# Optimization experiments

Measured on AMD Instinct MI355X. Metric: run time of the kernel, lower is better.

## Reference

```python
import jax, jax.numpy as jnp
import numpy as np

V, D, H, L, T_CTX = 50257, 768, 12, 12, 1024
HD = D // H
GELU_C = float(np.sqrt(2.0 / np.pi))


def new_gelu(x):
    return 0.5 * x * (1.0 + jnp.tanh(GELU_C * (x + 0.044715 * x ** 3)))


def layernorm(x, w, b, eps=1e-5):
    mu = jnp.mean(x, axis=-1, keepdims=True)
    var = jnp.var(x, axis=-1, keepdims=True)
    return (x - mu) * jax.lax.rsqrt(var + eps) * w + b


def setup_inputs() -> dict:
    key = jax.random.key(0)
    ks = jax.random.split(key, 20)
    B, T = 2, 1024
    s = 0.02
    inp = {
        "idx": jax.random.randint(ks[0], (B, T), 0, V),
        "targets": jax.random.randint(ks[1], (B, T), 0, V),
        "wte": jax.random.normal(ks[2], (V, D), jnp.float32) * s,
        "wpe": jax.random.normal(ks[3], (T_CTX, D), jnp.float32) * s,
        "ln1_w": jnp.ones((L, D)), "ln1_b": jnp.zeros((L, D)),
        "qkv_w": jax.random.normal(ks[4], (L, D, 3 * D), jnp.float32) * s,
        "qkv_b": jnp.zeros((L, 3 * D)),
        "proj_w": jax.random.normal(ks[5], (L, D, D), jnp.float32) * s,
        "proj_b": jnp.zeros((L, D)),
        "ln2_w": jnp.ones((L, D)), "ln2_b": jnp.zeros((L, D)),
        "fc_w": jax.random.normal(ks[6], (L, D, 4 * D), jnp.float32) * s,
        "fc_b": jnp.zeros((L, 4 * D)),
        "fc2_w": jax.random.normal(ks[7], (L, 4 * D, D), jnp.float32) * s,
        "fc2_b": jnp.zeros((L, D)),
        "lnf_w": jnp.ones((D,)), "lnf_b": jnp.zeros((D,)),
    }
    return inp


def _gpt_forward(idx, targets, wte, wpe, ln1_w, ln1_b, qkv_w, qkv_b, proj_w,
                 proj_b, ln2_w, ln2_b, fc_w, fc_b, fc2_w, fc2_b, lnf_w, lnf_b):
    B, T = idx.shape
    x = wte[idx] + wpe[:T]  # [B,T,D]
    scale = 1.0 / np.sqrt(HD)
    causal = jnp.tril(jnp.ones((T, T), dtype=bool))

    def block(x, p):
        l1w, l1b, qw, qb, pw, pb, l2w, l2b, fw, fb, f2w, f2b = p
        h = layernorm(x, l1w, l1b)
        qkv = h @ qw + qb  # [B,T,3D]
        q, k, v = jnp.split(qkv, 3, axis=-1)
        q = q.reshape(B, T, H, HD).transpose(0, 2, 1, 3)
        k = k.reshape(B, T, H, HD).transpose(0, 2, 1, 3)
        v = v.reshape(B, T, H, HD).transpose(0, 2, 1, 3)
        attn = jnp.einsum('bhqd,bhkd->bhqk', q, k) * scale
        attn = jnp.where(causal, attn, -jnp.inf)
        attn = jax.nn.softmax(attn, axis=-1)
        o = jnp.einsum('bhqk,bhkd->bhqd', attn, v)
        o = o.transpose(0, 2, 1, 3).reshape(B, T, D)
        x = x + (o @ pw + pb)
        h = layernorm(x, l2w, l2b)
        h = new_gelu(h @ fw + fb) @ f2w + f2b
        return x + h, None

    params = (ln1_w, ln1_b, qkv_w, qkv_b, proj_w, proj_b,
              ln2_w, ln2_b, fc_w, fc_b, fc2_w, fc2_b)
    x, _ = jax.lax.scan(block, x, params)
    x = layernorm(x, lnf_w, lnf_b)
    logits = x @ wte.T  # tied lm_head, [B,T,V]

    logp = jax.nn.log_softmax(logits, axis=-1)
    tflat = targets.reshape(-1)
    valid = tflat != -1
    tsafe = jnp.where(valid, tflat, 0)
    nll = -jnp.take_along_axis(logp.reshape(-1, V), tsafe[:, None], axis=-1)[:, 0]
    loss = jnp.sum(jnp.where(valid, nll, 0.0)) / jnp.maximum(jnp.sum(valid), 1)
    return logits, loss


def reference(idx, targets, wte, wpe, ln1_w, ln1_b, qkv_w, qkv_b, proj_w,
              proj_b, ln2_w, ln2_b, fc_w, fc_b, fc2_w, fc2_b, lnf_w, lnf_b):
    return _gpt_forward(idx, targets, wte, wpe, ln1_w, ln1_b, qkv_w, qkv_b,
                        proj_w, proj_b, ln2_w, ln2_b, fc_w, fc_b, fc2_w, fc2_b,
                        lnf_w, lnf_b)
```

## Files before the change

### kernel.cpp

```cpp
#include <hip/hip_runtime.h>
#include <hip/hip_bf16.h>
#include <math.h>

#define TT 1024
#define BB 2
#define DD 768
#define HH 12
#define NHD 64
#define LL 12
#define VV 50257
#define MROWS (BB*TT)
#define VPAD 50304

typedef __attribute__((ext_vector_type(4))) float f32x4;
typedef __attribute__((ext_vector_type(8))) __bf16 bf16x8;
typedef __attribute__((ext_vector_type(8))) unsigned short u16x8;
typedef __hip_bfloat16 bf16;

__device__ __forceinline__ void gload_lds16(const bf16* g, bf16* l) {
    __builtin_amdgcn_global_load_lds((const __attribute__((address_space(1))) void*)g,
                                     (__attribute__((address_space(3))) void*)l, 16, 0, 0);
}

__global__ void embed_kernel(const int* __restrict__ idx, const float* __restrict__ wte,
                             const float* __restrict__ wpe, float* __restrict__ x) {
    int m = blockIdx.x;
    int t = m % TT;
    int tok = idx[m];
    const float* wrow = wte + (size_t)tok * DD;
    const float* prow = wpe + (size_t)t * DD;
    float* xrow = x + (size_t)m * DD;
    for (int c = threadIdx.x; c < DD; c += blockDim.x)
        xrow[c] = wrow[c] + prow[c];
}

__global__ void ln_kernel(const float* __restrict__ x, const float* __restrict__ w,
                          const float* __restrict__ b, bf16* __restrict__ out) {
    __shared__ float red[256];
    int m = blockIdx.x;
    int tid = threadIdx.x;
    const float* xr = x + (size_t)m * DD;
    float v0 = xr[tid], v1 = xr[tid + 256], v2 = xr[tid + 512];
    red[tid] = v0 + v1 + v2;
    __syncthreads();
    for (int s = 128; s > 0; s >>= 1) { if (tid < s) red[tid] += red[tid + s]; __syncthreads(); }
    float mu = red[0] * (1.0f / DD);
    __syncthreads();
    float d0 = v0 - mu, d1 = v1 - mu, d2 = v2 - mu;
    red[tid] = d0 * d0 + d1 * d1 + d2 * d2;
    __syncthreads();
    for (int s = 128; s > 0; s >>= 1) { if (tid < s) red[tid] += red[tid + s]; __syncthreads(); }
    float rstd = rsqrtf(red[0] * (1.0f / DD) + 1e-5f);
    bf16* orow = out + (size_t)m * DD;
    orow[tid]       = __float2bfloat16(d0 * rstd * w[tid]       + b[tid]);
    orow[tid + 256] = __float2bfloat16(d1 * rstd * w[tid + 256] + b[tid + 256]);
    orow[tid + 512] = __float2bfloat16(d2 * rstd * w[tid + 512] + b[tid + 512]);
}

__global__ void cast_kernel(const float* __restrict__ src, bf16* __restrict__ dst, int n4) {
    int stride = gridDim.x * blockDim.x;
    for (int i = blockIdx.x * blockDim.x + threadIdx.x; i < n4; i += stride) {
        float4 v = *(const float4*)(src + (size_t)i * 4);
        bf16* d = dst + (size_t)i * 4;
        d[0] = __float2bfloat16(v.x); d[1] = __float2bfloat16(v.y);
        d[2] = __float2bfloat16(v.z); d[3] = __float2bfloat16(v.w);
    }
}

__global__ void tcast_kernel(const float* __restrict__ W, bf16* __restrict__ Wt,
                             int K, int N, size_t wstride, size_t tstride) {
    W  += (size_t)blockIdx.z * wstride;
    Wt += (size_t)blockIdx.z * tstride;
    __shared__ float t[32][33];
    int n0 = blockIdx.x * 32, k0 = blockIdx.y * 32;
    int c = threadIdx.x & 31, g = threadIdx.x >> 5;
    #pragma unroll
    for (int i = 0; i < 4; ++i) {
        int k = g * 4 + i;
        t[k][c] = W[(size_t)(k0 + k) * N + n0 + c];
    }
    __syncthreads();
    #pragma unroll
    for (int i = 0; i < 4; ++i) {
        int n = g * 4 + i;
        Wt[(size_t)(n0 + n) * K + k0 + c] = __float2bfloat16(t[c][n]);
    }
}

template<int BM, int BN, bool BIAS, bool GELU_, bool RES, bool OUTBF16, bool NCHECK, bool SPLITK>
__global__ __launch_bounds__(256, 3) void mgemm(
        const bf16* __restrict__ A, const bf16* __restrict__ Bm,
        const float* __restrict__ bias, const float* __restrict__ res,
        float* __restrict__ Cf, bf16* __restrict__ Cb, int M, int N, int K) {
    constexpr int WM = BM / 32, WN = BN / 32;
    constexpr int RA = BM / 64, RB = BN / 64;
    constexpr int NL = RA + RB;
    __shared__ __align__(16) bf16 As[2][BM * 32];
    __shared__ __align__(16) bf16 Bs[2][BN * 32];
    const int tid = threadIdx.x, lane = tid & 63, wid = tid >> 6;
    const int nbx = gridDim.x;
    const int nwg = nbx * gridDim.y;
    const int bidl = blockIdx.x + nbx * blockIdx.y;
    const int cpx = nwg >> 3;
    const int sw = (bidl & 7) * cpx + (bidl >> 3);
    const int m0 = (sw % nbx) * BM, n0 = (sw / nbx) * BN;
    const int wr = (wid >> 1) * (BM / 2), wc = (wid & 1) * (BN / 2);
    const int fr = lane & 15, fq = lane >> 4;

    const int Keff  = SPLITK ? (K >> 1) : K;
    const int kbase = SPLITK ? blockIdx.z * Keff : 0;
    if (SPLITK) Cf += (size_t)blockIdx.z * M * N;

    const int ksrc = ((lane & 3) ^ ((lane >> 3) & 3)) * 8;
    const bf16* gA = A  + (size_t)(m0 + wid * 16 + (lane >> 2)) * K + kbase + ksrc;
    const bf16* gB = Bm + (size_t)(n0 + wid * 16 + (lane >> 2)) * K + kbase + ksrc;
    bf16* lA = &As[0][0] + wid * 512 + lane * 8;
    bf16* lB = &Bs[0][0] + wid * 512 + lane * 8;
    const int kph = (fq ^ ((fr >> 1) & 3)) * 8;

    f32x4 acc[WM][WN] = {};
    const int nt = Keff / 32;

    #pragma unroll
    for (int i = 0; i < RA; ++i) gload_lds16(gA + (size_t)(i * 64) * K, lA + i * 2048);
    #pragma unroll
    for (int i = 0; i < RB; ++i) gload_lds16(gB + (size_t)(i * 64) * K, lB + i * 2048);

    for (int t = 0; t < nt; ++t) {
        const int cur = t & 1;
        if (t + 1 < nt) {
            const bf16* pA = gA + (t + 1) * 32;
            const bf16* pB = gB + (t + 1) * 32;
            bf16* dA = lA + (cur ^ 1) * (BM * 32);
            bf16* dB = lB + (cur ^ 1) * (BN * 32);
            #pragma unroll
            for (int i = 0; i < RA; ++i) gload_lds16(pA + (size_t)(i * 64) * K, dA + i * 2048);
            #pragma unroll
            for (int i = 0; i < RB; ++i) gload_lds16(pB + (size_t)(i * 64) * K, dB + i * 2048);
            asm volatile("s_waitcnt vmcnt(%0)" :: "i"(NL) : "memory");
        } else {
            asm volatile("s_waitcnt vmcnt(0)" ::: "memory");
        }
        __builtin_amdgcn_s_barrier();
        __builtin_amdgcn_sched_barrier(0);
        const bf16* abase = &As[cur][0];
        const bf16* bbase = &Bs[cur][0];
        bf16x8 af[WM], bq[WN];
        #pragma unroll
        for (int m = 0; m < WM; ++m)
            af[m] = *(const bf16x8*)(abase + (wr + m * 16 + fr) * 32 + kph);
        #pragma unroll
        for (int n = 0; n < WN; ++n)
            bq[n] = *(const bf16x8*)(bbase + (wc + n * 16 + fr) * 32 + kph);
        #pragma unroll
        for (int m = 0; m < WM; ++m)
            #pragma unroll
            for (int n = 0; n < WN; ++n)
                acc[m][n] = __builtin_amdgcn_mfma_f32_16x16x32_bf16(af[m], bq[n], acc[m][n], 0, 0, 0);
        __builtin_amdgcn_sched_barrier(0);
        __builtin_amdgcn_s_barrier();
    }

    #pragma unroll
    for (int m = 0; m < WM; ++m) {
        const int row = m0 + wr + m * 16 + fq * 4;
        #pragma unroll
        for (int n = 0; n < WN; ++n) {
            const int col = n0 + wc + n * 16 + fr;
            if (NCHECK && col >= N) continue;
            float bv = BIAS ? bias[col] : 0.f;
            #pragma unroll
            for (int r = 0; r < 4; ++r) {
                float v = acc[m][n][r] + bv;
                if (GELU_) {
                    float u = v;
                    v = 0.5f * u * (1.0f + tanhf(0.7978845608028654f * (u + 0.044715f * u * u * u)));
                }
                if (RES) v += res[(size_t)(row + r) * N + col];
                if (OUTBF16) Cb[(size_t)(row + r) * N + col] = __float2bfloat16(v);
                else         Cf[(size_t)(row + r) * N + col] = v;
            }
        }
    }
}

__global__ void red_kernel(const float* __restrict__ part, const float* __restrict__ bias,
                           float* __restrict__ x) {
    const size_t MN = (size_t)MROWS * DD;
    size_t i = ((size_t)blockIdx.x * blockDim.x + threadIdx.x) * 4;
    float4 p0 = *(const float4*)(part + i);
    float4 p1 = *(const float4*)(part + MN + i);
    float4 xv = *(const float4*)(x + i);
    float4 bv = *(const float4*)(bias + (int)(i % DD));
    xv.x += p0.x + p1.x + bv.x;
    xv.y += p0.y + p1.y + bv.y;
    xv.z += p0.z + p1.z + bv.z;
    xv.w += p0.w + p1.w + bv.w;
    *(float4*)(x + i) = xv;
}

__global__ __launch_bounds__(256) void attn3_kernel(const bf16* __restrict__ qkv,
                                                    bf16* __restrict__ out) {
    __shared__ bf16 Vt[64 * 64];
    __shared__ bf16 Ps[4][16 * 64];
    const int bid = blockIdx.x;
    const int q0 = (15 - (bid & 15)) * 64;
    const int h  = (bid / (TT / 64)) % HH;
    const int b  = bid / ((TT / 64) * HH);
    const int tid = threadIdx.x, lane = tid & 63, wid = tid >> 6;
    const int fr = lane & 15, fq = lane >> 4;
    const size_t rs = 3 * DD;

    bf16x8 qf[2];
    {
        const bf16* qb = qkv + (size_t)(b * TT + q0 + wid * 16 + fr) * rs + h * NHD;
        qf[0] = *(const bf16x8*)(qb + fq * 8);
        qf[1] = *(const bf16x8*)(qb + 32 + fq * 8);
    }
    float mrun[4] = {-1e30f, -1e30f, -1e30f, -1e30f};
    float lrun[4] = {0.f, 0.f, 0.f, 0.f};
    f32x4 o[4] = {};
    const int vrow = (tid & 31) * 2, kq = tid >> 5;
    const int ntile = q0 / 64 + 1;

    for (int jt = 0; jt < ntile; ++jt) {
        __syncthreads();
        {
            const u16x8* vb = (const u16x8*)(qkv + (size_t)(b * TT + jt * 64 + vrow) * rs + 2 * DD + h * NHD + kq * 8);
            u16x8 v0 = vb[0];
            u16x8 v1 = *(const u16x8*)((const bf16*)vb + rs);
            #pragma unroll
            for (int j = 0; j < 8; ++j) {
                int d = kq * 8 + j;
                int e = (d * 64 + vrow) ^ ((d & 7) << 3);
                *(unsigned int*)&Vt[e] = (unsigned int)v0[j] | ((unsigned int)v1[j] << 16);
            }
        }
        f32x4 s[4] = {};
        const bf16* kb = qkv + (size_t)(b * TT + jt * 64 + fr) * rs + DD + h * NHD;
        __builtin_amdgcn_s_setprio(1);
        #pragma unroll
        for (int n = 0; n < 4; ++n) {
            bf16x8 k0 = *(const bf16x8*)(kb + (size_t)(n * 16) * rs + fq * 8);
            bf16x8 k1 = *(const bf16x8*)(kb + (size_t)(n * 16) * rs + 32 + fq * 8);
            s[n] = __builtin_amdgcn_mfma_f32_16x16x32_bf16(qf[0], k0, s[n], 0, 0, 0);
            s[n] = __builtin_amdgcn_mfma_f32_16x16x32_bf16(qf[1], k1, s[n], 0, 0, 0);
        }
        __builtin_amdgcn_s_setprio(0);
        float mt[4] = {-1e30f, -1e30f, -1e30f, -1e30f};
        #pragma unroll
        for (int n = 0; n < 4; ++n) {
            int colg = jt * 64 + n * 16 + fr;
            #pragma unroll
            for (int r = 0; r < 4; ++r) {
                int rowg = q0 + wid * 16 + fq * 4 + r;
                float v = s[n][r] * 0.125f;
                if (colg > rowg) v = -1e30f;
                s[n][r] = v;
                mt[r] = fmaxf(mt[r], v);
            }
        }
        #pragma unroll
        for (int msk = 1; msk <= 8; msk <<= 1)
            #pragma unroll
            for (int r = 0; r < 4; ++r) mt[r] = fmaxf(mt[r], __shfl_xor(mt[r], msk));
        float sc[4], pt[4] = {0.f, 0.f, 0.f, 0.f};
        #pragma unroll
        for (int r = 0; r < 4; ++r) {
            float mn = fmaxf(mrun[r], mt[r]);
            sc[r] = __expf(mrun[r] - mn);
            mrun[r] = mn;
        }
        #pragma unroll
        for (int n = 0; n < 4; ++n)
            #pragma unroll
            for (int r = 0; r < 4; ++r) {
                float p = __expf(s[n][r] - mrun[r]);
                s[n][r] = p;
                pt[r] += p;
            }
        #pragma unroll
        for (int msk = 1; msk <= 8; msk <<= 1)
            #pragma unroll
            for (int r = 0; r < 4; ++r) pt[r] += __shfl_xor(pt[r], msk);
        #pragma unroll
        for (int r = 0; r < 4; ++r) lrun[r] = lrun[r] * sc[r] + pt[r];
        #pragma unroll
        for (int n2 = 0; n2 < 4; ++n2)
            #pragma unroll
            for (int r = 0; r < 4; ++r) o[n2][r] *= sc[r];
        #pragma unroll
        for (int n = 0; n < 4; ++n)
            #pragma unroll
            for (int r = 0; r < 4; ++r) {
                int row = fq * 4 + r;
                int e = (row * 64 + n * 16 + fr) ^ ((row & 7) << 3);
                Ps[wid][e] = __float2bfloat16(s[n][r]);
            }
        __syncthreads();
        __builtin_amdgcn_s_setprio(1);
        #pragma unroll
        for (int ks = 0; ks < 2; ++ks) {
            int pe = (fr * 64 + ks * 32 + fq * 8) ^ ((fr & 7) << 3);
            bf16x8 pa = *(const bf16x8*)&Ps[wid][pe];
            #pragma unroll
            for (int n2 = 0; n2 < 4; ++n2) {
                int d = n2 * 16 + fr;
                int ve = (d * 64 + ks * 32 + fq * 8) ^ ((d & 7) << 3);
                bf16x8 vv = *(const bf16x8*)&Vt[ve];
                o[n2] = __builtin_amdgcn_mfma_f32_16x16x32_bf16(pa, vv, o[n2], 0, 0, 0);
            }
        }
        __builtin_amdgcn_s_setprio(0);
    }
    #pragma unroll
    for (int r = 0; r < 4; ++r) {
        float inv = 1.f / lrun[r];
        bf16* op = out + (size_t)(b * TT + q0 + wid * 16 + fq * 4 + r) * DD + h * NHD;
        #pragma unroll
        for (int n2 = 0; n2 < 4; ++n2)
            op[n2 * 16 + fr] = __float2bfloat16(o[n2][r] * inv);
    }
}

__global__ void zero_kernel(float* p) { if (threadIdx.x == 0) p[0] = 0.f; }

__device__ __forceinline__ void ol_push(float v, float& mx, float& sm) {
    if (v > mx) { sm *= __expf(mx - v); mx = v; }
    sm += __expf(v - mx);
}

__global__ void loss_kernel(const float* __restrict__ logits, const int* __restrict__ targets,
                            float* __restrict__ acc) {
    __shared__ float rm[256], rs[256];
    int m = blockIdx.x;
    int tid = threadIdx.x;
    const float* lr = logits + (size_t)m * VV;
    const int lead = (4 - (m & 3)) & 3;
    const int nv = (VV - lead) >> 2;
    float mx = -1e30f, sm = 0.f;
    if (tid < lead) ol_push(lr[tid], mx, sm);
    const float4* lr4 = (const float4*)(lr + lead);
    for (int i = tid; i < nv; i += 256) {
        float4 v = lr4[i];
        ol_push(v.x, mx, sm); ol_push(v.y, mx, sm);
        ol_push(v.z, mx, sm); ol_push(v.w, mx, sm);
    }
    for (int i = lead + 4 * nv + tid; i < VV; i += 256) ol_push(lr[i], mx, sm);
    rm[tid] = mx; rs[tid] = sm;
    __syncthreads();
    for (int s = 128; s > 0; s >>= 1) {
        if (tid < s) {
            float m2 = rm[tid + s], s2 = rs[tid + s];
            float nm = fmaxf(rm[tid], m2);
            rs[tid] = rs[tid] * __expf(rm[tid] - nm) + s2 * __expf(m2 - nm);
            rm[tid] = nm;
        }
        __syncthreads();
    }
    if (tid == 0) {
        float lse = logf(rs[0]) + rm[0];
        atomicAdd(acc, lse - lr[targets[m]]);
    }
}

__global__ void loss_final(const float* __restrict__ acc, float* __restrict__ out) {
    if (threadIdx.x == 0) out[0] = acc[0] * (1.0f / (float)MROWS);
}

extern "C" void kernel_launch(void* const* d_in, const int* in_sizes, int n_in,
                              void* d_out, int out_size, void* d_ws, size_t ws_size,
                              hipStream_t stream) {
    const int*   idx     = (const int*)d_in[0];
    const int*   targets = (const int*)d_in[1];
    const float* wte     = (const float*)d_in[2];
    const float* wpe     = (const float*)d_in[3];
    const float* ln1_w   = (const float*)d_in[4];
    const float* ln1_b   = (const float*)d_in[5];
    const float* qkv_w   = (const float*)d_in[6];
    const float* qkv_b   = (const float*)d_in[7];
    const float* proj_w  = (const float*)d_in[8];
    const float* proj_b  = (const float*)d_in[9];
    const float* ln2_w   = (const float*)d_in[10];
    const float* ln2_b   = (const float*)d_in[11];
    const float* fc_w    = (const float*)d_in[12];
    const float* fc_b    = (const float*)d_in[13];
    const float* fc2_w   = (const float*)d_in[14];
    const float* fc2_b   = (const float*)d_in[15];
    const float* lnf_w   = (const float*)d_in[16];
    const float* lnf_b   = (const float*)d_in[17];

    float* logits = (float*)d_out;
    float* loss_out = logits + (size_t)MROWS * VV;

    const size_t LQ = (size_t)3 * DD * DD, LP = (size_t)DD * DD;
    const size_t LF = (size_t)4 * DD * DD, LF2 = (size_t)4 * DD * DD;
    const size_t LSTRIDE = LQ + LP + LF + LF2;

    float* x    = (float*)d_ws;
    float* lacc = x + (size_t)MROWS * DD;
    float* part = lacc + 16;
    bf16* qkvbuf = (bf16*)(part + (size_t)2 * MROWS * DD);
    bf16* hb   = qkvbuf + (size_t)MROWS * 3 * DD;
    bf16* ab   = hb + (size_t)MROWS * DD;
    bf16* gb   = ab + (size_t)MROWS * DD;
    bf16* wteb = gb + (size_t)MROWS * 4 * DD;
    bf16* wbase = wteb + (size_t)VPAD * DD;

    const size_t fixed_bytes = (size_t)((char*)wbase - (char*)d_ws);
    const bool hoist = ws_size >= fixed_bytes + sizeof(bf16) * LSTRIDE * LL;

    dim3 blk(256);
    cast_kernel<<<2048, blk, 0, stream>>>(wte, wteb, VV * DD / 4);
    embed_kernel<<<MROWS, blk, 0, stream>>>(idx, wte, wpe, x);

    if (hoist) {
        tcast_kernel<<<dim3(3 * DD / 32, DD / 32, LL), blk, 0, stream>>>(
            qkv_w, wbase, DD, 3 * DD, LQ, LSTRIDE);
        tcast_kernel<<<dim3(DD / 32, DD / 32, LL), blk, 0, stream>>>(
            proj_w, wbase + LQ, DD, DD, LP, LSTRIDE);
        tcast_kernel<<<dim3(4 * DD / 32, DD / 32, LL), blk, 0, stream>>>(
            fc_w, wbase + LQ + LP, DD, 4 * DD, LF, LSTRIDE);
        tcast_kernel<<<dim3(DD / 32, 4 * DD / 32, LL), blk, 0, stream>>>(
            fc2_w, wbase + LQ + LP + LF, 4 * DD, DD, LF2, LSTRIDE);
    }

    const int nred = (MROWS * DD) / (4 * 256);

    for (int l = 0; l < LL; ++l) {
        bf16* wl = hoist ? wbase + (size_t)l * LSTRIDE : wbase;
        bf16* wQT = wl, *wPT = wl + LQ, *wFT = wl + LQ + LP, *wF2T = wl + LQ + LP + LF;
        if (!hoist) {
            tcast_kernel<<<dim3(3 * DD / 32, DD / 32, 1), blk, 0, stream>>>(qkv_w + (size_t)l * LQ, wQT, DD, 3 * DD, 0, 0);
            tcast_kernel<<<dim3(DD / 32, DD / 32, 1), blk, 0, stream>>>(proj_w + (size_t)l * LP, wPT, DD, DD, 0, 0);
            tcast_kernel<<<dim3(4 * DD / 32, DD / 32, 1), blk, 0, stream>>>(fc_w + (size_t)l * LF, wFT, DD, 4 * DD, 0, 0);
            tcast_kernel<<<dim3(DD / 32, 4 * DD / 32, 1), blk, 0, stream>>>(fc2_w + (size_t)l * LF2, wF2T, 4 * DD, DD, 0, 0);
        }

        ln_kernel<<<MROWS, blk, 0, stream>>>(x, ln1_w + (size_t)l * DD, ln1_b + (size_t)l * DD, hb);

        mgemm<128, 128, true, false, false, true, false, false><<<dim3(MROWS / 128, 3 * DD / 128), blk, 0, stream>>>(
            hb, wQT, qkv_b + (size_t)l * 3 * DD, nullptr, nullptr, qkvbuf, MROWS, 3 * DD, DD);

        attn3_kernel<<<BB * HH * (TT / 64), blk, 0, stream>>>(qkvbuf, ab);

        mgemm<64, 64, false, false, false, false, false, true><<<dim3(MROWS / 64, DD / 64, 2), blk, 0, stream>>>(
            ab, wPT, nullptr, nullptr, part, nullptr, MROWS, DD, DD);
        red_kernel<<<nred, blk, 0, stream>>>(part, proj_b + (size_t)l * DD, x);

        ln_kernel<<<MROWS, blk, 0, stream>>>(x, ln2_w + (size_t)l * DD, ln2_b + (size_t)l * DD, hb);

        mgemm<128, 128, true, true, false, true, false, false><<<dim3(MROWS / 128, 4 * DD / 128), blk, 0, stream>>>(
            hb, wFT, fc_b + (size_t)l * 4 * DD, nullptr, nullptr, gb, MROWS, 4 * DD, DD);

        mgemm<64, 64, false, false, false, false, false, true><<<dim3(MROWS / 64, DD / 64, 2), blk, 0, stream>>>(
            gb, wF2T, nullptr, nullptr, part, nullptr, MROWS, DD, 4 * DD);
        red_kernel<<<nred, blk, 0, stream>>>(part, fc2_b + (size_t)l * DD, x);
    }

    ln_kernel<<<MROWS, blk, 0, stream>>>(x, lnf_w, lnf_b, hb);

    mgemm<128, 128, false, false, false, false, true, false><<<dim3(MROWS / 128, VPAD / 128), blk, 0, stream>>>(
        hb, wteb, nullptr, nullptr, logits, nullptr, MROWS, VV, DD);

    zero_kernel<<<1, 64, 0, stream>>>(lacc);
    loss_kernel<<<MROWS, blk, 0, stream>>>(logits, targets, lacc);
    loss_final<<<1, 64, 0, stream>>>(lacc, loss_out);
}
```

Before: 2.567 ms.

## Use 256x256-tile double-buffered MFMA GEMM with XCD swizzle for lm_head

Replaces the 128x128 generic GEMM for the tied lm_head projection with a dedicated 512-thread, 256x256-tile kernel. It uses swizzled LDS layout, direct global-to-LDS loads interleaved between MFMA groups, setprio, and a block-index remap that groups workgroups by XCD. The vocab padding grows to a multiple of 256, and the pad rows are zeroed by a new kernel. The aim is higher arithmetic intensity and better MFMA utilisation on the largest GEMM, at the cost of heavier LDS use (128KB per block) and more complex manual waitcnt scheduling.

```diff
diff --git a/kernel.cpp b/kernel.cpp
--- a/kernel.cpp
+++ b/kernel.cpp
@@ -10,7 +10,7 @@
 #define LL 12
 #define VV 50257
 #define MROWS (BB*TT)
-#define VPAD 50304
+#define NPAD 50432
 
 typedef __attribute__((ext_vector_type(4))) float f32x4;
 typedef __attribute__((ext_vector_type(8))) __bf16 bf16x8;
@@ -67,6 +67,11 @@
     }
 }
 
+__global__ void padzero_kernel(bf16* __restrict__ p, int n) {
+    int i = blockIdx.x * 256 + threadIdx.x;
+    if (i < n) p[i] = __float2bfloat16(0.f);
+}
+
 __global__ void tcast_kernel(const float* __restrict__ W, bf16* __restrict__ Wt,
                              int K, int N, size_t wstride, size_t tstride) {
     W  += (size_t)blockIdx.z * wstride;
@@ -179,6 +184,94 @@
                 if (RES) v += res[(size_t)(row + r) * N + col];
                 if (OUTBF16) Cb[(size_t)(row + r) * N + col] = __float2bfloat16(v);
                 else         Cf[(size_t)(row + r) * N + col] = v;
+            }
+        }
+    }
+}
+
+template<int K>
+__global__ __launch_bounds__(512, 2) void mgemm256(
+        const bf16* __restrict__ A, const bf16* __restrict__ Bm,
+        float* __restrict__ Cf, int N) {
+    __shared__ __align__(16) bf16 As[2][256 * 64];
+    __shared__ __align__(16) bf16 Bs[2][256 * 64];
+    const int tid = threadIdx.x, lane = tid & 63, wid = tid >> 6;
+    const int wm = wid >> 2, wn = wid & 3;
+    const int fr = lane & 15, fq = lane >> 4;
+    const int nbx = gridDim.x;
+    const int nwg = nbx * gridDim.y;
+    const int bidl = blockIdx.x + nbx * blockIdx.y;
+    const int cpx = nwg >> 3;
+    const int sw = (bidl & 7) * cpx + (bidl >> 3);
+    const int m0 = (sw % nbx) * 256, n0 = (sw / nbx) * 256;
+
+    const int srow = tid >> 3;
+    const int ksw  = ((tid & 7) ^ (srow & 7)) * 8;
+    const int nt = K / 64;
+    const int swl = fr & 7;
+
+    f32x4 acc[8][4] = {};
+
+#define STA(T, U) gload_lds16(A  + (size_t)(m0 + (U)*64 + srow) * K + (T)*64 + ksw, \
+                              &As[(T) & 1][0] + (U)*4096 + tid*8)
+#define STB(T, U) gload_lds16(Bm + (size_t)(n0 + (U)*64 + srow) * K + (T)*64 + ksw, \
+                              &Bs[(T) & 1][0] + (U)*4096 + tid*8)
+#define LDA(DST, M_, KS) DST = *(const bf16x8*)(ab + (wm*128 + (M_)*16 + fr)*64 + ((((KS)*4+fq) ^ swl)*8))
+#define LDB(DST, N_, KS) DST = *(const bf16x8*)(bb + (wn*64  + (N_)*16 + fr)*64 + ((((KS)*4+fq) ^ swl)*8))
+#define MFMA16(Q) { bf16x8 a0, a1, a2, a3;                                         \
+        LDA(a0, 2*(Q),   0); LDA(a1, 2*(Q),   1);                                  \
+        LDA(a2, 2*(Q)+1, 0); LDA(a3, 2*(Q)+1, 1);                                  \
+        __builtin_amdgcn_s_setprio(1);                                             \
+        _Pragma("unroll")                                                          \
+        for (int n = 0; n < 4; ++n) {                                              \
+            acc[2*(Q)][n]   = __builtin_amdgcn_mfma_f32_16x16x32_bf16(a0, bq[n][0], acc[2*(Q)][n], 0, 0, 0);   \
+            acc[2*(Q)][n]   = __builtin_amdgcn_mfma_f32_16x16x32_bf16(a1, bq[n][1], acc[2*(Q)][n], 0, 0, 0);   \
+            acc[2*(Q)+1][n] = __builtin_amdgcn_mfma_f32_16x16x32_bf16(a2, bq[n][0], acc[2*(Q)+1][n], 0, 0, 0); \
+            acc[2*(Q)+1][n] = __builtin_amdgcn_mfma_f32_16x16x32_bf16(a3, bq[n][1], acc[2*(Q)+1][n], 0, 0, 0); \
+        }                                                                          \
+        __builtin_amdgcn_s_setprio(0); }
+
+    STA(0,0); STA(0,1); STA(0,2); STA(0,3); STB(0,0); STB(0,1); STB(0,2); STB(0,3);
+    STA(1,0); STA(1,1); STA(1,2); STA(1,3); STB(1,0); STB(1,1); STB(1,2); STB(1,3);
+
+    #pragma unroll 1
+    for (int t = 0; t < nt; ++t) {
+        const bf16* ab = &As[t & 1][0];
+        const bf16* bb = &Bs[t & 1][0];
+        if (t + 1 < nt) asm volatile("s_waitcnt vmcnt(6)" ::: "memory");
+        else            asm volatile("s_waitcnt vmcnt(0)" ::: "memory");
+        __builtin_amdgcn_s_barrier();
+        if (t >= 1 && t + 1 < nt) { STA(t+1, 1); STA(t+1, 3); }
+        bf16x8 bq[4][2];
+        #pragma unroll
+        for (int n = 0; n < 4; ++n) { LDB(bq[n][0], n, 0); LDB(bq[n][1], n, 1); }
+        MFMA16(0)
+        __builtin_amdgcn_s_barrier();
+        if (t + 2 < nt) { STB(t+2, 0); STB(t+2, 1); }
+        MFMA16(1)
+        __builtin_amdgcn_s_barrier();
+        if (t + 2 < nt) { STB(t+2, 2); STB(t+2, 3); STA(t+2, 0); STA(t+2, 2); }
+        MFMA16(2)
+        __builtin_amdgcn_s_barrier();
+        MFMA16(3)
+        __builtin_amdgcn_s_barrier();
+    }
+#undef STA
+#undef STB
+#undef LDA
+#undef LDB
+#undef MFMA16
+
+    #pragma unroll
+    for (int m = 0; m < 8; ++m) {
+        const int row = m0 + wm * 128 + m * 16 + fq * 4;
+        #pragma unroll
+        for (int n = 0; n < 4; ++n) {
+            const int col = n0 + wn * 64 + n * 16 + fr;
+            if (col < N) {
+                #pragma unroll
+                for (int r = 0; r < 4; ++r)
+                    Cf[(size_t)(row + r) * N + col] = acc[m][n][r];
             }
         }
     }
@@ -405,13 +498,15 @@
     bf16* ab   = hb + (size_t)MROWS * DD;
     bf16* gb   = ab + (size_t)MROWS * DD;
     bf16* wteb = gb + (size_t)MROWS * 4 * DD;
-    bf16* wbase = wteb + (size_t)VPAD * DD;
+    bf16* wbase = wteb + (size_t)NPAD * DD;
 
     const size_t fixed_bytes = (size_t)((char*)wbase - (char*)d_ws);
     const bool hoist = ws_size >= fixed_bytes + sizeof(bf16) * LSTRIDE * LL;
 
     dim3 blk(256);
     cast_kernel<<<2048, blk, 0, stream>>>(wte, wteb, VV * DD / 4);
+    padzero_kernel<<<((NPAD - VV) * DD + 255) / 256, blk, 0, stream>>>(
+        wteb + (size_t)VV * DD, (NPAD - VV) * DD);
     embed_kernel<<<MROWS, blk, 0, stream>>>(idx, wte, wpe, x);
 
     if (hoist) {
@@ -460,8 +555,8 @@
 
     ln_kernel<<<MROWS, blk, 0, stream>>>(x, lnf_w, lnf_b, hb);
 
-    mgemm<128, 128, false, false, false, false, true, false><<<dim3(MROWS / 128, VPAD / 128), blk, 0, stream>>>(
-        hb, wteb, nullptr, nullptr, logits, nullptr, MROWS, VV, DD);
+    mgemm256<DD><<<dim3(MROWS / 256, NPAD / 256), dim3(512), 0, stream>>>(
+        hb, wteb, logits, VV);
 
     zero_kernel<<<1, 64, 0, stream>>>(lacc);
     loss_kernel<<<MROWS, blk, 0, stream>>>(logits, targets, lacc);
```

New measurement: 2.601 ms. No clear change (+1.3%).
